# Optimization experiments

Measured on AMD Instinct MI355X. Metric: run time of the kernel, lower is better.

Reference implementation:

```python
import jax, jax.numpy as jnp
import numpy as np

SHIFT = 1  # module picks shift_direction in {-1,+1} at init via random(); fixed to +1


def setup_inputs() -> dict:
    key = jax.random.key(0)
    kx, kw = jax.random.split(key)
    x = jax.random.normal(kx, (128, 128, 28, 28), dtype=jnp.float32)  # (B, Cin, H, W)
    w = jax.random.normal(kw, (32, 128, 3), dtype=jnp.float32)        # (Cout, Cin, K)
    return {"x": x, "w": w}


def reference(x, w):
    # The unfold+einsum in the original is a conv1d over the last (W) axis with
    # kernel 3, padding 1; the H axis is untouched. Express it as a 2D conv with
    # a (1,3) kernel so no im2col buffer is materialized.
    y = jax.lax.conv_general_dilated(
        x, w[:, :, None, :],                     # kernel (Cout, Cin, 1, 3)
        window_strides=(1, 1),
        padding=((0, 0), (1, 1)),
        dimension_numbers=("NCHW", "OIHW", "NCHW"))  # -> (B, 32, H, W)
    # Original rolls the H axis (after moving it next to batch) by shift_direction.
    return jnp.roll(y, SHIFT, axis=2)
```

## Files before the change

### kernel.cpp

```cpp
#include <hip/hip_runtime.h>


#define CIN   128
#define COUT  32
#define HH    28
#define WW    28
#define CIP   136
#define WPD   34
#define HROWS 2
#define NTHR  128

typedef __attribute__((ext_vector_type(8))) short short8;
typedef __attribute__((ext_vector_type(8))) __bf16 bf16x8;
typedef __attribute__((ext_vector_type(16))) float f32x16;

__device__ inline unsigned short f2bf(float f) {
    union { float f; unsigned u; } v; v.f = f;
    return (unsigned short)((v.u + 0x7FFFu + ((v.u >> 16) & 1u)) >> 16);
}

__device__ inline unsigned int pack_bf2(float a, float b) {
#if __has_builtin(__builtin_amdgcn_cvt_pk_bf16_f32)
    typedef __attribute__((ext_vector_type(2))) __bf16 bf16x2;
    bf16x2 t = __builtin_amdgcn_cvt_pk_bf16_f32(a, b);
    return __builtin_bit_cast(unsigned int, t);
#else
    return (unsigned)f2bf(a) | ((unsigned)f2bf(b) << 16);
#endif
}

__global__ void build_wfrag(const float* __restrict__ wt, unsigned short* __restrict__ wf) {
    int t = blockIdx.x * 256 + threadIdx.x;
    if (t >= 24 * 64 * 8) return;
    int j = t & 7, lane = (t >> 3) & 63, s = t >> 9;
    int co = lane & 31;
    int k  = s * 16 + (lane >> 5) * 8 + j;
    int kk = k >> 7, ci = k & 127;
    wf[t] = f2bf(wt[((size_t)co * CIN + ci) * 3 + kk]);
}

__global__ __launch_bounds__(NTHR, 3) void conv_mfma(
    const float* __restrict__ x,
    const unsigned short* __restrict__ wf,
    float* __restrict__ out)
{
    __shared__ __align__(16) unsigned short xt[HROWS][WPD][CIP];

    const int tid = threadIdx.x;
    const int hp  = blockIdx.x;
    const int b   = blockIdx.y;
    const int h0  = hp * HROWS;
    const float* xb = x + (size_t)b * CIN * HH * WW;

    {
        unsigned int* xu = (unsigned int*)xt;
        const int ROWU = CIP / 2;
        for (int i = tid; i < 4 * ROWU; i += NTHR) {
            int row = i / ROWU;
            int hl  = row & 1;
            int wp  = (row >> 1) ? 29 : 0;
            xu[(hl * WPD + wp) * ROWU + (i % ROWU)] = 0u;
        }
    }

#pragma unroll
    for (int p = 0; p < 7; ++p) {
        int q   = tid + p * NTHR;
        int w4  = q % 7;
        int r   = q / 7;
        int hl  = r & 1;
        int ci0 = (r >> 1) * 2;
        const float* base = xb + ((size_t)ci0 * HH + (h0 + hl)) * WW + w4 * 4;
        float4 v0 = *(const float4*)(base);
        float4 v1 = *(const float4*)(base + HH * WW);
        int wp = 1 + w4 * 4;
        *(unsigned int*)&xt[hl][wp + 0][ci0] = pack_bf2(v0.x, v1.x);
        *(unsigned int*)&xt[hl][wp + 1][ci0] = pack_bf2(v0.y, v1.y);
        *(unsigned int*)&xt[hl][wp + 2][ci0] = pack_bf2(v0.z, v1.z);
        *(unsigned int*)&xt[hl][wp + 3][ci0] = pack_bf2(v0.w, v1.w);
    }

    __syncthreads();

    const int lane = tid & 63;
    const int hl   = tid >> 6;
    const int n    = lane & 31;
    const int half = lane >> 5;
    f32x16 acc = {0,0,0,0,0,0,0,0,0,0,0,0,0,0,0,0};

#pragma unroll
    for (int kk = 0; kk < 3; ++kk) {
        short8 afr[8];
#pragma unroll
        for (int u = 0; u < 8; ++u)
            afr[u] = *(const short8*)(wf + (size_t)((kk * 8 + u) * 64 + lane) * 8);
#pragma unroll
        for (int u = 0; u < 8; ++u) {
            short8 bfr = *(const short8*)&xt[hl][n + kk][u * 16 + half * 8];
            acc = __builtin_amdgcn_mfma_f32_32x32x16_bf16(
                __builtin_bit_cast(bf16x8, afr[u]),
                __builtin_bit_cast(bf16x8, bfr), acc, 0, 0, 0);
        }
    }

    if (n < WW) {
        const int hout = (h0 + hl + 1) % HH;
#pragma unroll
        for (int r = 0; r < 16; ++r) {
            int co = (r & 3) + 8 * (r >> 2) + 4 * half;
            out[(((size_t)b * COUT + co) * HH + hout) * WW + n] = acc[r];
        }
    }
}

extern "C" void kernel_launch(void* const* d_in, const int* in_sizes, int n_in,
                              void* d_out, int out_size, void* d_ws, size_t ws_size,
                              hipStream_t stream) {
    const float* x  = (const float*)d_in[0];
    const float* wt = (const float*)d_in[1];
    float* out = (float*)d_out;
    unsigned short* wf = (unsigned short*)d_ws;

    build_wfrag<<<48, 256, 0, stream>>>(wt, wf);
    dim3 grid(HH / HROWS, 128);
    conv_mfma<<<grid, NTHR, 0, stream>>>(x, wf, out);
}
```

Measured before the change: 94.23 us.

## Fuse weight fragment build into conv kernel and process four rows per block

Removes the separate weight-preparation kernel launch: each block now reads the fp32 weights directly, converts them to bf16 and scatters them into an MFMA-fragment layout in shared memory, then reads A fragments from LDS instead of global memory. The tile grows to four H rows and 256 threads per block, which halves the grid and spreads the per-block weight conversion over more output work. In exchange, every block redoes the weight conversion and LDS use rises by about 24 KB for the weight buffer, lowering occupancy.

```diff
diff --git a/kernel.cpp b/kernel.cpp
--- a/kernel.cpp
+++ b/kernel.cpp
@@ -7,14 +7,14 @@
 #define WW    28
 #define CIP   136
 #define WPD   34
-#define HROWS 2
-#define NTHR  128
+#define HROWS 4
+#define NTHR  256
 
 typedef __attribute__((ext_vector_type(8))) short short8;
 typedef __attribute__((ext_vector_type(8))) __bf16 bf16x8;
 typedef __attribute__((ext_vector_type(16))) float f32x16;
 
-__device__ inline unsigned short f2bf(float f) {
+__device__ inline unsigned short f2bf_sw(float f) {
     union { float f; unsigned u; } v; v.f = f;
     return (unsigned short)((v.u + 0x7FFFu + ((v.u >> 16) & 1u)) >> 16);
 }
@@ -25,40 +25,53 @@
     bf16x2 t = __builtin_amdgcn_cvt_pk_bf16_f32(a, b);
     return __builtin_bit_cast(unsigned int, t);
 #else
-    return (unsigned)f2bf(a) | ((unsigned)f2bf(b) << 16);
+    return (unsigned)f2bf_sw(a) | ((unsigned)f2bf_sw(b) << 16);
 #endif
 }
 
-__global__ void build_wfrag(const float* __restrict__ wt, unsigned short* __restrict__ wf) {
-    int t = blockIdx.x * 256 + threadIdx.x;
-    if (t >= 24 * 64 * 8) return;
-    int j = t & 7, lane = (t >> 3) & 63, s = t >> 9;
-    int co = lane & 31;
-    int k  = s * 16 + (lane >> 5) * 8 + j;
-    int kk = k >> 7, ci = k & 127;
-    wf[t] = f2bf(wt[((size_t)co * CIN + ci) * 3 + kk]);
+__device__ inline unsigned short f2bf1(float a) {
+    return (unsigned short)(pack_bf2(a, a) & 0xFFFFu);
 }
 
-__global__ __launch_bounds__(NTHR, 3) void conv_mfma(
+__global__ __launch_bounds__(NTHR, 2) void conv_fused(
     const float* __restrict__ x,
-    const unsigned short* __restrict__ wf,
+    const float* __restrict__ wt,
     float* __restrict__ out)
 {
+    __shared__ __align__(16) unsigned short wfl[24 * 64 * 8];
     __shared__ __align__(16) unsigned short xt[HROWS][WPD][CIP];
 
     const int tid = threadIdx.x;
-    const int hp  = blockIdx.x;
+    const int hq  = blockIdx.x;
     const int b   = blockIdx.y;
-    const int h0  = hp * HROWS;
+    const int h0  = hq * HROWS;
     const float* xb = x + (size_t)b * CIN * HH * WW;
+
+#pragma unroll
+    for (int it = 0; it < 12; ++it) {
+        int p0 = (tid + it * NTHR) * 4;
+        float4 v = *(const float4*)(wt + p0);
+        float vv[4] = {v.x, v.y, v.z, v.w};
+#pragma unroll
+        for (int e = 0; e < 4; ++e) {
+            int p  = p0 + e;
+            int kk = p % 3, c = p / 3;
+            int co = c >> 7, ci = c & 127;
+            int k  = kk * 128 + ci;
+            int s  = k >> 4;
+            int lane = ((k >> 3) & 1) * 32 + co;
+            int j  = k & 7;
+            wfl[(s * 64 + lane) * 8 + j] = f2bf1(vv[e]);
+        }
+    }
 
     {
         unsigned int* xu = (unsigned int*)xt;
         const int ROWU = CIP / 2;
-        for (int i = tid; i < 4 * ROWU; i += NTHR) {
+        for (int i = tid; i < HROWS * 2 * ROWU; i += NTHR) {
             int row = i / ROWU;
-            int hl  = row & 1;
-            int wp  = (row >> 1) ? 29 : 0;
+            int hl  = row >> 1;
+            int wp  = (row & 1) ? 29 : 0;
             xu[(hl * WPD + wp) * ROWU + (i % ROWU)] = 0u;
         }
     }
@@ -68,8 +81,8 @@
         int q   = tid + p * NTHR;
         int w4  = q % 7;
         int r   = q / 7;
-        int hl  = r & 1;
-        int ci0 = (r >> 1) * 2;
+        int hl  = r & 3;
+        int ci0 = (r >> 2) * 2;
         const float* base = xb + ((size_t)ci0 * HH + (h0 + hl)) * WW + w4 * 4;
         float4 v0 = *(const float4*)(base);
         float4 v1 = *(const float4*)(base + HH * WW);
@@ -90,15 +103,12 @@
 
 #pragma unroll
     for (int kk = 0; kk < 3; ++kk) {
-        short8 afr[8];
-#pragma unroll
-        for (int u = 0; u < 8; ++u)
-            afr[u] = *(const short8*)(wf + (size_t)((kk * 8 + u) * 64 + lane) * 8);
 #pragma unroll
         for (int u = 0; u < 8; ++u) {
+            short8 afr = *(const short8*)&wfl[((kk * 8 + u) * 64 + lane) * 8];
             short8 bfr = *(const short8*)&xt[hl][n + kk][u * 16 + half * 8];
             acc = __builtin_amdgcn_mfma_f32_32x32x16_bf16(
-                __builtin_bit_cast(bf16x8, afr[u]),
+                __builtin_bit_cast(bf16x8, afr),
                 __builtin_bit_cast(bf16x8, bfr), acc, 0, 0, 0);
         }
     }
@@ -119,9 +129,6 @@
     const float* x  = (const float*)d_in[0];
     const float* wt = (const float*)d_in[1];
     float* out = (float*)d_out;
-    unsigned short* wf = (unsigned short*)d_ws;
-
-    build_wfrag<<<48, 256, 0, stream>>>(wt, wf);
     dim3 grid(HH / HROWS, 128);
-    conv_mfma<<<grid, NTHR, 0, stream>>>(x, wf, out);
+    conv_fused<<<grid, NTHR, 0, stream>>>(x, wt, out);
 }
```

New measurement: 95.02 us. No clear change (+0.8%).
